# Kernel optimization log

Measured on AMD Instinct MI355X. Metric: run time of the kernel, lower is better.

Reference implementation:

```python
import jax, jax.numpy as jnp
import numpy as np

N_CLASSES = 80
TOPK = 13
ALPHA = 1.0
BETA = 6.0
EPS = 1e-9
BS, N_ANCHORS, N_MAX = 32, 8400, 100


def setup_inputs() -> dict:
    key = jax.random.key(0)
    k1, k2, k3, k4, k5, k6 = jax.random.split(key, 6)
    pred_scores = jax.random.uniform(k1, (BS, N_ANCHORS, N_CLASSES), dtype=jnp.float32)
    anchor_points = jax.random.uniform(k2, (N_ANCHORS, 2), dtype=jnp.float32) * 640.0
    # predicted boxes centered on anchor points (valid xyxy)
    wh = jax.random.uniform(k3, (BS, N_ANCHORS, 2), dtype=jnp.float32) * 100.0 + 4.0
    ctr = anchor_points[None]
    pred_bboxes = jnp.concatenate([ctr - wh / 2, ctr + wh / 2], axis=-1)
    gt_lt = jax.random.uniform(k4, (BS, N_MAX, 2), dtype=jnp.float32) * 500.0
    gt_wh = jax.random.uniform(k5, (BS, N_MAX, 2), dtype=jnp.float32) * 120.0 + 8.0
    gt_bboxes = jnp.concatenate([gt_lt, gt_lt + gt_wh], axis=-1)
    gt_labels = jax.random.randint(k6, (BS, N_MAX, 1), 0, N_CLASSES).astype(jnp.int32)
    mask_gt = jnp.ones((BS, N_MAX, 1), dtype=jnp.float32)
    return {"pred_scores": pred_scores, "pred_bboxes": pred_bboxes,
            "anchor_points": anchor_points, "gt_labels": gt_labels,
            "gt_bboxes": gt_bboxes, "mask_gt": mask_gt}


def _batch_iou(a, b):
    # a: [bs, n, 4], b: [bs, m, 4] (xyxy) -> [bs, n, m]
    lt = jnp.maximum(a[:, :, None, :2], b[:, None, :, :2])
    rb = jnp.minimum(a[:, :, None, 2:], b[:, None, :, 2:])
    wh = jnp.clip(rb - lt, 0.0)
    inter = wh[..., 0] * wh[..., 1]
    area_a = ((a[..., 2] - a[..., 0]) * (a[..., 3] - a[..., 1]))[:, :, None]
    area_b = ((b[..., 2] - b[..., 0]) * (b[..., 3] - b[..., 1]))[:, None, :]
    return inter / (area_a + area_b - inter + EPS)


def _assign(pred_scores, pred_bboxes, anchor_points, gt_labels, gt_bboxes, mask_gt):
    bs, n_anchors, n_classes = pred_scores.shape
    n_max = gt_bboxes.shape[1]
    labels = gt_labels[..., 0].astype(jnp.int32)  # [bs, n_max]

    # alignment metric: bbox_scores[b,g,a] = pred_scores[b,a,labels[b,g]]
    ps_t = jnp.swapaxes(pred_scores, 1, 2)  # [bs, C, n_anchors]
    bbox_scores = jnp.take_along_axis(ps_t, labels[:, :, None], axis=1)  # [bs, n_max, n_anchors]
    overlaps = _batch_iou(gt_bboxes, pred_bboxes)  # [bs, n_max, n_anchors]
    align_metric = jnp.power(bbox_scores, ALPHA) * jnp.power(overlaps, BETA)

    # anchor centers inside gt boxes
    ap = anchor_points[None, None, :, :]  # [1,1,n_anchors,2]
    deltas = jnp.concatenate(
        [ap - gt_bboxes[:, :, None, :2], gt_bboxes[:, :, None, 2:] - ap], axis=-1)
    is_in_gts = (deltas.min(axis=-1) > EPS).astype(align_metric.dtype)  # [bs,n_max,n_anchors]

    # topk candidate selection
    metrics = align_metric * is_in_gts
    _, topk_idxs = jax.lax.top_k(metrics, TOPK)  # [bs, n_max, TOPK]
    topk_mask = (mask_gt > 0)  # [bs, n_max, 1], broadcasts over TOPK
    topk_idxs = jnp.where(topk_mask, topk_idxs, 0)

    def count_row(idx):  # idx: [TOPK] -> anchor hit counts [n_anchors]
        return jnp.zeros((n_anchors,), jnp.int32).at[idx].add(1)
    counts = jax.vmap(jax.vmap(count_row))(topk_idxs)  # [bs, n_max, n_anchors]
    is_in_topk = jnp.where(counts > 1, 0, counts).astype(metrics.dtype)

    mask_pos = is_in_topk * is_in_gts * mask_gt  # [bs, n_max, n_anchors]

    # fix collisions: anchors assigned to multiple GTs keep the max-IoU GT
    mask_pos_sum = mask_pos.sum(axis=1)  # [bs, n_anchors]
    multi = mask_pos_sum[:, None, :] > 1
    is_max_overlaps = jax.nn.one_hot(overlaps.argmax(axis=1), n_max, axis=1,
                                     dtype=mask_pos.dtype)  # [bs, n_max, n_anchors]
    mask_pos = jnp.where(multi, is_max_overlaps, mask_pos)
    mask_pos_sum = mask_pos.sum(axis=1)
    assigned_gt_idx = mask_pos.argmax(axis=1)  # [bs, n_anchors]

    # final assignments via flattened gather
    flat_idx = assigned_gt_idx + jnp.arange(bs, dtype=jnp.int32)[:, None] * n_max
    assigned_labels = labels.reshape(-1)[flat_idx]  # [bs, n_anchors]
    assigned_bboxes = gt_bboxes.reshape(-1, 4)[flat_idx]  # [bs, n_anchors, 4]
    assigned_labels = jnp.where(assigned_labels < 0, 0, assigned_labels)
    assigned_scores = jax.nn.one_hot(assigned_labels, n_classes, dtype=pred_scores.dtype)
    pos = mask_pos_sum > 0
    assigned_scores = jnp.where(pos[..., None], assigned_scores, 0.0)
    assigned_labels = jnp.where(pos, assigned_labels, n_classes)

    # normalize scores by alignment metric
    align_metric = align_metric * mask_pos
    pos_align = align_metric.max(axis=-1, keepdims=True)  # [bs, n_max, 1]
    pos_overlaps = (overlaps * mask_pos).max(axis=-1, keepdims=True)
    norm = (align_metric * pos_overlaps / (pos_align + EPS)).max(axis=1)[..., None]  # [bs,n_anchors,1]
    assigned_scores = assigned_scores * norm

    return assigned_labels, assigned_bboxes, assigned_scores, pos


def reference(pred_scores, pred_bboxes, anchor_points, gt_labels, gt_bboxes, mask_gt):
    return _assign(pred_scores, pred_bboxes, anchor_points, gt_labels, gt_bboxes, mask_gt)
```

## Files before the change

### kernel.cpp

```cpp
#include <hip/hip_runtime.h>

#define BS 32
#define NA 8400
#define NMAX 100
#define NC 80
#define TOPK 13
#define EPSF 1e-9f
#define WCAP 1024
#define NSTRIP 64
#define STRIP_INV 0.1f

#define OFF_LBL  0
#define OFF_BOX  (BS*NA)
#define OFF_SCR  (BS*NA + BS*NA*4)
#define OFF_POS  (BS*NA + BS*NA*4 + BS*NA*NC)

#define NROWS (BS*NMAX)
#define NSC4  (BS*NA*NC/4)
#define ZBLK  511
#define NCHUNK 33
#define NWID  (BS*NCHUNK*4)

__global__ __launch_bounds__(1024) void bin_zero_kernel(
    const float* __restrict__ anchor_points,
    int* __restrict__ strip_off, float4* __restrict__ sAPI,
    unsigned int* __restrict__ pz_base,
    float* __restrict__ out)
{
    int t = threadIdx.x;
    if (blockIdx.x != 0) {
        int zb = blockIdx.x - 1;
        if (zb == 0) {
            uint4* pz = (uint4*)pz_base;
            uint4 zz = make_uint4(0u, 0u, 0u, 0u);
            for (int i = t; i < 1600; i += 1024) pz[i] = zz;
        }
        float4* sz = (float4*)(out + OFF_SCR);
        float4 zf = make_float4(0.f, 0.f, 0.f, 0.f);
        for (int i = zb * 1024 + t; i < NSC4; i += ZBLK * 1024) sz[i] = zf;
        return;
    }

    __shared__ int cnt[NSTRIP];
    __shared__ int cur[NSTRIP];
    if (t < NSTRIP) cnt[t] = 0;
    __syncthreads();
    const float2* ap2 = (const float2*)anchor_points;
    for (int a = t; a < NA; a += 1024) {
        int s = (int)(ap2[a].y * STRIP_INV);
        s = s < 0 ? 0 : (s > NSTRIP - 1 ? NSTRIP - 1 : s);
        atomicAdd(&cnt[s], 1);
    }
    __syncthreads();
    if (t < 64) {
        int v = cnt[t];
        int inc = v;
        #pragma unroll
        for (int d = 1; d < 64; d <<= 1) {
            int o = __shfl_up(inc, d, 64);
            if (t >= d) inc += o;
        }
        int excl = inc - v;
        cur[t] = excl; strip_off[t] = excl;
        if (t == 63) strip_off[64] = inc;
    }
    __syncthreads();
    for (int a = t; a < NA; a += 1024) {
        float2 p = ap2[a];
        int s = (int)(p.y * STRIP_INV);
        s = s < 0 ? 0 : (s > NSTRIP - 1 ? NSTRIP - 1 : s);
        int pos = atomicAdd(&cur[s], 1);
        sAPI[pos] = make_float4(p.x, p.y, __int_as_float(a), 0.f);
    }
}

__global__ __launch_bounds__(256) void topk_kernel(
    const float* __restrict__ pred_scores,
    const float* __restrict__ pred_bboxes,
    const int*   __restrict__ gt_labels,
    const float* __restrict__ gt_bboxes,
    const float* __restrict__ mask_gt,
    const int*   __restrict__ strip_off,
    const float4* __restrict__ sAPI,
    unsigned int*   __restrict__ ccount,
    unsigned short* __restrict__ clist)
{
    __shared__ unsigned short aidx[4][WCAP];
    int t = threadIdx.x;
    int wave = t >> 6;
    int lane = t & 63;
    int row = blockIdx.x * 4 + wave;
    if (mask_gt[row] <= 0.f) {
        if (lane == 0) ccount[row] = 0u;
        return;
    }
    int b = row / NMAX;

    const float* gbp = gt_bboxes + (size_t)row * 4;
    float gx1 = gbp[0], gy1 = gbp[1], gx2 = gbp[2], gy2 = gbp[3];
    int lab = gt_labels[row];

    int s_lo = (int)(gy1 * STRIP_INV); s_lo = s_lo < 0 ? 0 : (s_lo > NSTRIP-1 ? NSTRIP-1 : s_lo);
    int s_hi = (int)(gy2 * STRIP_INV); s_hi = s_hi < 0 ? 0 : (s_hi > NSTRIP-1 ? NSTRIP-1 : s_hi);
    int lo = strip_off[s_lo], hi = strip_off[s_hi + 1];

    int cnt = 0;
    for (int base = lo; base < hi; base += 64) {
        int p = base + lane;
        bool hit = false; int a = 0;
        if (p < hi) {
            float4 ap = sAPI[p];
            a = __float_as_int(ap.z);
            hit = (ap.x - gx1 > EPSF) && (ap.y - gy1 > EPSF) &&
                  (gx2 - ap.x > EPSF) && (gy2 - ap.y > EPSF);
        }
        unsigned long long mb = __ballot(hit);
        if (hit) {
            int my = cnt + __popcll(mb & ((1ULL << lane) - 1ULL));
            if (my < WCAP) aidx[wave][my] = (unsigned short)a;
        }
        cnt += __popcll(mb);
    }
    if (cnt > WCAP) cnt = WCAP;

    unsigned long long loc[TOPK];
    #pragma unroll
    for (int i = 0; i < TOPK; i++) loc[i] = 0ULL;
    const float4* pb4 = (const float4*)pred_bboxes;
    for (int p = lane; p < cnt; p += 64) {
        int a = aidx[wave][p];
        float4 pb = pb4[b * NA + a];
        float s = pred_scores[((size_t)b * NA + a) * NC + lab];
        float lx = fmaxf(gx1, pb.x), ly = fmaxf(gy1, pb.y);
        float rx = fminf(gx2, pb.z), ry = fminf(gy2, pb.w);
        float w = fmaxf(rx - lx, 0.f), h = fmaxf(ry - ly, 0.f);
        float inter = w * h;
        float aa = (gx2 - gx1) * (gy2 - gy1);
        float ab = (pb.z - pb.x) * (pb.w - pb.y);
        float iou = inter / (aa + ab - inter + EPSF);
        float i2 = iou * iou;
        float m = s * (i2 * i2 * i2);
        if (m > 0.f) {
            unsigned long long key =
                ((unsigned long long)__float_as_uint(m) << 32) |
                (unsigned int)(NA - a);
            #pragma unroll
            for (int i = 0; i < TOPK; i++) {
                if (key > loc[i]) { unsigned long long tmp = loc[i]; loc[i] = key; key = tmp; }
            }
        }
    }

    int picks = TOPK;
    for (int r = 0; r < TOPK; r++) {
        unsigned long long h = loc[0];
        unsigned long long m = h;
        #pragma unroll
        for (int s = 32; s > 0; s >>= 1) {
            unsigned long long o = __shfl_xor(m, s, 64);
            m = o > m ? o : m;
        }
        if (m == 0ULL) { picks = r; break; }
        unsigned long long ball = __ballot(h == m);
        if (lane == (int)__builtin_ctzll(ball)) {
            #pragma unroll
            for (int i = 0; i < TOPK - 1; i++) loc[i] = loc[i + 1];
            loc[TOPK - 1] = 0ULL;
            int a = NA - (int)(unsigned int)(m & 0xFFFFFFFFULL);
            clist[row * TOPK + r] = (unsigned short)a;
        }
    }
    if (lane == 0) ccount[row] = (unsigned int)picks;
}

__global__ __launch_bounds__(256) void resolve_kernel(
    const float* __restrict__ pred_scores,
    const float* __restrict__ pred_bboxes,
    const int*   __restrict__ gt_labels,
    const float* __restrict__ gt_bboxes,
    const unsigned int*   __restrict__ ccount,
    const unsigned short* __restrict__ clist,
    unsigned int* __restrict__ pa_bits, unsigned int* __restrict__ po_bits,
    unsigned int* __restrict__ wcount, uint4* __restrict__ plist,
    float* __restrict__ out)
{
    __shared__ float4 gtb[NMAX];
    __shared__ int    glab[NMAX];
    __shared__ int    ccnt[NMAX];
    __shared__ unsigned int pkl[256];
    int b = blockIdx.y;
    int t = threadIdx.x;
    int lane = t & 63;
    int lo = blockIdx.x * 256;
    int ai = lo + t;
    bool valid = ai < NA;
    int idx = b * NA + (valid ? ai : 0);

    float4 pb = ((const float4*)pred_bboxes)[idx];

    if (t < NMAX) {
        gtb[t]  = ((const float4*)gt_bboxes)[b * NMAX + t];
        glab[t] = gt_labels[b * NMAX + t];
        ccnt[t] = (int)ccount[b * NMAX + t];
    }
    pkl[t] = 0u;
    __syncthreads();

    for (int e = t; e < NMAX * TOPK; e += 256) {
        int j = e / TOPK, k = e - j * TOPK;
        if (k < ccnt[j]) {
            int a = clist[(b * NMAX + j) * TOPK + k];
            unsigned int w = (unsigned int)(a - lo);
            if (w < 256u) atomicAdd(&pkl[w], (1u << 16) | (unsigned int)j);
        }
    }
    __syncthreads();

    unsigned int pk = valid ? pkl[t] : 0u;
    int js = -1; float iou = 0.f;

    if ((pk >> 16) == 1u) {
        js = (int)(pk & 0xFFFFu);
        float4 g = gtb[js];
        float lx = fmaxf(g.x, pb.x), ly = fmaxf(g.y, pb.y);
        float rx = fminf(g.z, pb.z), ry = fminf(g.w, pb.w);
        float w = fmaxf(rx - lx, 0.f), h = fmaxf(ry - ly, 0.f);
        float inter = w * h;
        float aa = (g.z - g.x) * (g.w - g.y);
        float ab = (pb.z - pb.x) * (pb.w - pb.y);
        iou = inter / (aa + ab - inter + EPSF);
    }

    unsigned long long mm = __ballot((pk >> 16) > 1u);
    while (mm) {
        int src = (int)__builtin_ctzll(mm);
        mm &= mm - 1ULL;
        float qx1 = __shfl(pb.x, src, 64), qy1 = __shfl(pb.y, src, 64);
        float qx2 = __shfl(pb.z, src, 64), qy2 = __shfl(pb.w, src, 64);
        float qab = (qx2 - qx1) * (qy2 - qy1);
        unsigned long long bestkey = 0ULL;
        #pragma unroll
        for (int rep = 0; rep < 2; rep++) {
            int j = lane + rep * 64;
            if (j < NMAX) {
                float4 g = gtb[j];
                float lx = fmaxf(g.x, qx1), ly = fmaxf(g.y, qy1);
                float rx = fminf(g.z, qx2), ry = fminf(g.w, qy2);
                float w = fmaxf(rx - lx, 0.f), h = fmaxf(ry - ly, 0.f);
                float inter = w * h;
                float aa = (g.z - g.x) * (g.w - g.y);
                float v = inter / (aa + qab - inter + EPSF);
                unsigned long long key =
                    ((unsigned long long)__float_as_uint(v) << 32) |
                    (unsigned int)(NMAX - 1 - j);
                if (key > bestkey) bestkey = key;
            }
        }
        #pragma unroll
        for (int s = 32; s > 0; s >>= 1) {
            unsigned long long o = __shfl_xor(bestkey, s, 64);
            bestkey = o > bestkey ? o : bestkey;
        }
        if (lane == src) {
            js  = NMAX - 1 - (int)(unsigned int)(bestkey & 0xFFFFFFFFULL);
            iou = __uint_as_float((unsigned int)(bestkey >> 32));
        }
    }

    float align = 0.f; int lab = 0;
    if (js >= 0) {
        lab = glab[js];
        float s = pred_scores[(size_t)idx * NC + lab];
        float i2 = iou * iou;
        align = s * (i2 * i2 * i2);
        atomicMax(&pa_bits[b * NMAX + js], __float_as_uint(align));
        atomicMax(&po_bits[b * NMAX + js], __float_as_uint(iou));
    }

    if (valid) {
        bool pos = js >= 0;
        int j0 = pos ? js : 0;
        out[OFF_LBL + idx] = pos ? (float)glab[j0] : (float)NC;
        ((float4*)(out + OFF_BOX))[idx] = gtb[j0];
        out[OFF_POS + idx] = pos ? 1.f : 0.f;
    }

    bool pos = valid && js >= 0;
    unsigned long long mb = __ballot(pos);
    int wid = (b * NCHUNK + blockIdx.x) * 4 + (t >> 6);
    if (lane == 0) wcount[wid] = (unsigned int)__popcll(mb);
    if (pos) {
        int myoff = __popcll(mb & ((1ULL << lane) - 1ULL));
        plist[wid * 64 + myoff] = make_uint4((unsigned int)idx,
                                             (unsigned int)(b * NMAX + js),
                                             __float_as_uint(align),
                                             (unsigned int)lab);
    }
}

__global__ __launch_bounds__(256) void scatter_kernel(
    const unsigned int* __restrict__ wcount, const uint4* __restrict__ plist,
    const unsigned int* __restrict__ pa_bits, const unsigned int* __restrict__ po_bits,
    float* __restrict__ out)
{
    int wid = blockIdx.x * 4 + (threadIdx.x >> 6);
    int lane = threadIdx.x & 63;
    unsigned int n = wcount[wid];
    if ((unsigned int)lane < n) {
        uint4 e = plist[wid * 64 + lane];
        float pa = __uint_as_float(pa_bits[e.y]);
        float po = __uint_as_float(po_bits[e.y]);
        out[OFF_SCR + (size_t)e.x * NC + e.w] = __uint_as_float(e.z) * po / (pa + EPSF);
    }
}

extern "C" void kernel_launch(void* const* d_in, const int* in_sizes, int n_in,
                              void* d_out, int out_size, void* d_ws, size_t ws_size,
                              hipStream_t stream) {
    const float* pred_scores   = (const float*)d_in[0];
    const float* pred_bboxes   = (const float*)d_in[1];
    const float* anchor_points = (const float*)d_in[2];
    const int*   gt_labels     = (const int*)d_in[3];
    const float* gt_bboxes     = (const float*)d_in[4];
    const float* mask_gt       = (const float*)d_in[5];

    char* ws = (char*)d_ws;
    unsigned int*   pa_bits = (unsigned int*)(ws);
    unsigned int*   po_bits = (unsigned int*)(ws + 12800);
    unsigned int*   ccount  = (unsigned int*)(ws + 25600);
    unsigned short* clist   = (unsigned short*)(ws + 38400);
    int*    strip_off = (int*)(ws + 121600);
    float4* sAPI      = (float4*)(ws + 122112);
    unsigned int* wcount = (unsigned int*)(ws + 256512);
    uint4*  plist     = (uint4*)(ws + 273408);

    float* out = (float*)d_out;

    bin_zero_kernel<<<1 + ZBLK, 1024, 0, stream>>>(
        anchor_points, strip_off, sAPI, pa_bits, out);

    topk_kernel<<<NROWS / 4, 256, 0, stream>>>(
        pred_scores, pred_bboxes, gt_labels, gt_bboxes, mask_gt,
        strip_off, sAPI, ccount, clist);

    dim3 rgrid(NCHUNK, BS);
    resolve_kernel<<<rgrid, 256, 0, stream>>>(
        pred_scores, pred_bboxes, gt_labels, gt_bboxes, ccount, clist,
        pa_bits, po_bits, wcount, plist, out);

    scatter_kernel<<<NWID / 4, 256, 0, stream>>>(
        wcount, plist, pa_bits, po_bits, out);
}
```

Baseline: 200.8 us.

## Move score zeroing into topk kernel and fuse scatter via last-block counter

```diff
diff --git a/kernel.cpp b/kernel.cpp
--- a/kernel.cpp
+++ b/kernel.cpp
@@ -17,27 +17,21 @@
 
 #define NROWS (BS*NMAX)
 #define NSC4  (BS*NA*NC/4)
-#define ZBLK  511
+#define TKBLK 800
+#define ZBLK2 1024
 #define NCHUNK 33
-#define NWID  (BS*NCHUNK*4)
-
-__global__ __launch_bounds__(1024) void bin_zero_kernel(
+#define WPB (NCHUNK*4)
+
+__global__ __launch_bounds__(1024) void bin_kernel(
     const float* __restrict__ anchor_points,
     int* __restrict__ strip_off, float4* __restrict__ sAPI,
-    unsigned int* __restrict__ pz_base,
-    float* __restrict__ out)
+    unsigned int* __restrict__ pz_base)
 {
     int t = threadIdx.x;
     if (blockIdx.x != 0) {
-        int zb = blockIdx.x - 1;
-        if (zb == 0) {
-            uint4* pz = (uint4*)pz_base;
-            uint4 zz = make_uint4(0u, 0u, 0u, 0u);
-            for (int i = t; i < 1600; i += 1024) pz[i] = zz;
-        }
-        float4* sz = (float4*)(out + OFF_SCR);
-        float4 zf = make_float4(0.f, 0.f, 0.f, 0.f);
-        for (int i = zb * 1024 + t; i < NSC4; i += ZBLK * 1024) sz[i] = zf;
+        uint4* pz = (uint4*)pz_base;
+        uint4 zz = make_uint4(0u, 0u, 0u, 0u);
+        for (int i = t; i < 1728; i += 1024) pz[i] = zz;
         return;
     }
 
@@ -83,10 +77,19 @@
     const int*   __restrict__ strip_off,
     const float4* __restrict__ sAPI,
     unsigned int*   __restrict__ ccount,
-    unsigned short* __restrict__ clist)
+    unsigned short* __restrict__ clist,
+    float* __restrict__ out)
 {
+    int t = threadIdx.x;
+    if (blockIdx.x >= TKBLK) {
+        int zb = blockIdx.x - TKBLK;
+        float4* sz = (float4*)(out + OFF_SCR);
+        float4 zf = make_float4(0.f, 0.f, 0.f, 0.f);
+        for (int i = zb * 256 + t; i < NSC4; i += ZBLK2 * 256) sz[i] = zf;
+        return;
+    }
+
     __shared__ unsigned short aidx[4][WCAP];
-    int t = threadIdx.x;
     int wave = t >> 6;
     int lane = t & 63;
     int row = blockIdx.x * 4 + wave;
@@ -181,6 +184,7 @@
     const unsigned int*   __restrict__ ccount,
     const unsigned short* __restrict__ clist,
     unsigned int* __restrict__ pa_bits, unsigned int* __restrict__ po_bits,
+    unsigned int* __restrict__ done,
     unsigned int* __restrict__ wcount, uint4* __restrict__ plist,
     float* __restrict__ out)
 {
@@ -188,6 +192,7 @@
     __shared__ int    glab[NMAX];
     __shared__ int    ccnt[NMAX];
     __shared__ unsigned int pkl[256];
+    __shared__ int lastflag;
     int b = blockIdx.y;
     int t = threadIdx.x;
     int lane = t & 63;
@@ -287,7 +292,7 @@
 
     bool pos = valid && js >= 0;
     unsigned long long mb = __ballot(pos);
-    int wid = (b * NCHUNK + blockIdx.x) * 4 + (t >> 6);
+    int wid = b * WPB + blockIdx.x * 4 + (t >> 6);
     if (lane == 0) wcount[wid] = (unsigned int)__popcll(mb);
     if (pos) {
         int myoff = __popcll(mb & ((1ULL << lane) - 1ULL));
@@ -296,21 +301,27 @@
                                              __float_as_uint(align),
                                              (unsigned int)lab);
     }
-}
-
-__global__ __launch_bounds__(256) void scatter_kernel(
-    const unsigned int* __restrict__ wcount, const uint4* __restrict__ plist,
-    const unsigned int* __restrict__ pa_bits, const unsigned int* __restrict__ po_bits,
-    float* __restrict__ out)
-{
-    int wid = blockIdx.x * 4 + (threadIdx.x >> 6);
-    int lane = threadIdx.x & 63;
-    unsigned int n = wcount[wid];
-    if ((unsigned int)lane < n) {
-        uint4 e = plist[wid * 64 + lane];
-        float pa = __uint_as_float(pa_bits[e.y]);
-        float po = __uint_as_float(po_bits[e.y]);
-        out[OFF_SCR + (size_t)e.x * NC + e.w] = __uint_as_float(e.z) * po / (pa + EPSF);
+
+    __threadfence();
+    __syncthreads();
+    if (t == 0) {
+        unsigned int old = atomicAdd(&done[b * 16], 1u);
+        lastflag = (old == (unsigned int)(NCHUNK - 1));
+    }
+    __syncthreads();
+    if (lastflag) {
+        __threadfence();
+        for (int slot = t; slot < WPB * 64; slot += 256) {
+            int w = slot >> 6;
+            unsigned int n = wcount[b * WPB + w];
+            if ((unsigned int)(slot & 63) < n) {
+                uint4 e = plist[(b * WPB + w) * 64 + (slot & 63)];
+                float pa = __uint_as_float(pa_bits[e.y]);
+                float po = __uint_as_float(po_bits[e.y]);
+                out[OFF_SCR + (size_t)e.x * NC + e.w] =
+                    __uint_as_float(e.z) * po / (pa + EPSF);
+            }
+        }
     }
 }
 
@@ -327,27 +338,25 @@
     char* ws = (char*)d_ws;
     unsigned int*   pa_bits = (unsigned int*)(ws);
     unsigned int*   po_bits = (unsigned int*)(ws + 12800);
-    unsigned int*   ccount  = (unsigned int*)(ws + 25600);
-    unsigned short* clist   = (unsigned short*)(ws + 38400);
-    int*    strip_off = (int*)(ws + 121600);
-    float4* sAPI      = (float4*)(ws + 122112);
-    unsigned int* wcount = (unsigned int*)(ws + 256512);
-    uint4*  plist     = (uint4*)(ws + 273408);
+    unsigned int*   done    = (unsigned int*)(ws + 25600);
+    unsigned int*   ccount  = (unsigned int*)(ws + 27648);
+    unsigned short* clist   = (unsigned short*)(ws + 40448);
+    int*    strip_off = (int*)(ws + 123648);
+    float4* sAPI      = (float4*)(ws + 124160);
+    unsigned int* wcount = (unsigned int*)(ws + 258560);
+    uint4*  plist     = (uint4*)(ws + 275456);
 
     float* out = (float*)d_out;
 
-    bin_zero_kernel<<<1 + ZBLK, 1024, 0, stream>>>(
-        anchor_points, strip_off, sAPI, pa_bits, out);
-
-    topk_kernel<<<NROWS / 4, 256, 0, stream>>>(
+    bin_kernel<<<2, 1024, 0, stream>>>(
+        anchor_points, strip_off, sAPI, pa_bits);
+
+    topk_kernel<<<TKBLK + ZBLK2, 256, 0, stream>>>(
         pred_scores, pred_bboxes, gt_labels, gt_bboxes, mask_gt,
-        strip_off, sAPI, ccount, clist);
+        strip_off, sAPI, ccount, clist, out);
 
     dim3 rgrid(NCHUNK, BS);
     resolve_kernel<<<rgrid, 256, 0, stream>>>(
         pred_scores, pred_bboxes, gt_labels, gt_bboxes, ccount, clist,
-        pa_bits, po_bits, wcount, plist, out);
-
-    scatter_kernel<<<NWID / 4, 256, 0, stream>>>(
-        wcount, plist, pa_bits, po_bits, out);
+        pa_bits, po_bits, done, wcount, plist, out);
 }
```

Measured after the change: 340.4 us. +69.5%, slower.
